# Performance work log

Hardware: AMD Instinct MI355X
Metric: run time of the kernel (lower is better)

Reference implementation:

```python
import jax, jax.numpy as jnp
import numpy as np

N_BAND = 5  # module hardcodes self.n = 5 -> keeps |i-j| <= N_BAND-1 = 4


def setup_inputs() -> dict:
    key = jax.random.key(0)
    ks = jax.random.split(key, 6)
    B, L, H = 4, 2048, 1024
    s = 1.0 / np.sqrt(H)
    return {
        "q": jax.random.normal(ks[0], (B, L, H), jnp.float32),
        "k": jax.random.normal(ks[1], (B, L, H), jnp.float32),
        "Wq": jax.random.normal(ks[2], (H, H), jnp.float32) * s,
        "bq": jax.random.normal(ks[3], (H,), jnp.float32) * s,
        "Wk": jax.random.normal(ks[4], (H, H), jnp.float32) * s,
        "bk": jax.random.normal(ks[5], (H,), jnp.float32) * s,
    }


def reference(q, k, Wq, bq, Wk, bk):
    b, l, e = q.shape
    # nn.Linear: y = x @ W^T + b
    qs = jnp.einsum("ble,he->blh", q, Wq) + bq
    ks = jnp.einsum("ble,he->blh", k, Wk) + bk
    # dense QK^T logits, [b, l, l]
    logits = jnp.einsum("blh,bmh->blm", qs, ks)
    # banded mask: the torch loop zeroes offsets 0..n-1 on both sides -> |i-j| <= n-1
    idx = jnp.arange(l)
    band = jnp.abs(idx[:, None] - idx[None, :]) <= (N_BAND - 1)  # [l, l]
    neg_inf = jnp.array(-jnp.inf, dtype=logits.dtype)
    logits = jnp.where(band[None, :, :], logits, neg_inf)
    # every row contains its diagonal, so softmax is well-defined
    return jax.nn.softmax(logits, axis=-1)
```

## Files before the change

kernel.cpp:

```cpp
#include <hip/hip_runtime.h>
#include <math.h>

#define LSEQ 2048
#define HDIM 1024
#define BATCH 4
#define ROWS (BATCH * LSEQ)
#define NBAND 9

typedef __attribute__((ext_vector_type(8))) short bf16x8;
typedef __attribute__((ext_vector_type(4))) float f32x4;
typedef __attribute__((ext_vector_type(8))) unsigned short u16x8;
typedef __attribute__((ext_vector_type(4))) unsigned uintx4;

#define AS3 __attribute__((address_space(3)))
#define AS1 __attribute__((address_space(1)))

__device__ __forceinline__ void gload16(const void* gp, void* lp) {
    __builtin_amdgcn_global_load_lds((AS1 const unsigned*)gp, (AS3 unsigned*)lp, 16, 0, 0);
}

__device__ __forceinline__ unsigned short f2bf(float x) {
    unsigned u = __float_as_uint(x);
    u += 0x7FFFu + ((u >> 16) & 1u);
    return (unsigned short)(u >> 16);
}
__device__ __forceinline__ float bf2f(unsigned short h) {
    return __uint_as_float(((unsigned)h) << 16);
}

__device__ __forceinline__ void split8(float4 a, float4 b, bf16x8& hi, bf16x8& lo) {
    float v[8] = {a.x, a.y, a.z, a.w, b.x, b.y, b.z, b.w};
#pragma unroll
    for (int j = 0; j < 8; j++) {
        unsigned short h = f2bf(v[j]);
        hi[j] = (short)h;
        lo[j] = (short)f2bf(v[j] - bf2f(h));
    }
}

__device__ __forceinline__ void unpack8(uintx4 w0, uintx4 w1, bf16x8& hi, bf16x8& lo) {
    union { bf16x8 v; uintx4 u; } H, L;
    H.u[0] = __builtin_amdgcn_perm(w0[1], w0[0], 0x05040100u);
    H.u[1] = __builtin_amdgcn_perm(w0[3], w0[2], 0x05040100u);
    H.u[2] = __builtin_amdgcn_perm(w1[1], w1[0], 0x05040100u);
    H.u[3] = __builtin_amdgcn_perm(w1[3], w1[2], 0x05040100u);
    L.u[0] = __builtin_amdgcn_perm(w0[1], w0[0], 0x07060302u);
    L.u[1] = __builtin_amdgcn_perm(w0[3], w0[2], 0x07060302u);
    L.u[2] = __builtin_amdgcn_perm(w1[1], w1[0], 0x07060302u);
    L.u[3] = __builtin_amdgcn_perm(w1[3], w1[2], 0x07060302u);
    hi = H.v; lo = L.v;
}

__global__ __launch_bounds__(256) void tcw_kernel(const float* __restrict__ Wq,
                                                  const float* __restrict__ Wk,
                                                  const float* __restrict__ bq,
                                                  unsigned short* __restrict__ qhi,
                                                  unsigned short* __restrict__ qlo,
                                                  unsigned short* __restrict__ khi,
                                                  unsigned short* __restrict__ klo,
                                                  float* __restrict__ wpart) {
    const int z = blockIdx.z;
    const int tid = threadIdx.x;
    if (z == 2) {
        const int fid = blockIdx.y * 16 + blockIdx.x;
        if (fid >= 64) return;
        const int c0 = tid * 4;
        float4 acc = {0.f, 0.f, 0.f, 0.f};
#pragma unroll
        for (int hh = 0; hh < 16; hh++) {
            const int h = fid * 16 + hh;
            const float s = bq[h];
            float4 v = *reinterpret_cast<const float4*>(&Wk[(size_t)h * HDIM + c0]);
            acc.x += v.x * s; acc.y += v.y * s; acc.z += v.z * s; acc.w += v.w * s;
        }
        *reinterpret_cast<float4*>(&wpart[(size_t)fid * HDIM + c0]) = acc;
        return;
    }
    __shared__ float tile[64][65];
    const float* src = z ? Wk : Wq;
    unsigned short* dh = z ? khi : qhi;
    unsigned short* dl = z ? klo : qlo;
    const int n0 = blockIdx.x * 64;
    const int h0 = blockIdx.y * 64;

#pragma unroll
    for (int p = 0; p < 4; p++) {
        const int h = p * 16 + (tid >> 4);
        const int n = (tid & 15) * 4;
        float4 v = *reinterpret_cast<const float4*>(&src[(size_t)(h0 + h) * HDIM + n0 + n]);
        tile[h][n + 0] = v.x; tile[h][n + 1] = v.y; tile[h][n + 2] = v.z; tile[h][n + 3] = v.w;
    }
    __syncthreads();
#pragma unroll
    for (int p = 0; p < 2; p++) {
        const int n = p * 32 + (tid >> 3);
        const int h = (tid & 7) * 8;
        u16x8 hv, lv;
#pragma unroll
        for (int j = 0; j < 8; j++) {
            float x = tile[h + j][n];
            unsigned short hb = f2bf(x);
            hv[j] = hb;
            lv[j] = f2bf(x - bf2f(hb));
        }
        *reinterpret_cast<u16x8*>(&dh[(size_t)(n0 + n) * HDIM + h0 + h]) = hv;
        *reinterpret_cast<u16x8*>(&dl[(size_t)(n0 + n) * HDIM + h0 + h]) = lv;
    }
}

__global__ __launch_bounds__(256) void convert_k_beta(const float* __restrict__ k,
                                                      const float* __restrict__ w,
                                                      unsigned short* __restrict__ Xhi,
                                                      unsigned short* __restrict__ Xlo,
                                                      float* __restrict__ beta) {
    __shared__ float red[4];
    const int r = blockIdx.x;
    const int t = threadIdx.x;
    float4 v = *reinterpret_cast<const float4*>(&k[(size_t)r * HDIM + t * 4]);
    float4 wv = *reinterpret_cast<const float4*>(&w[t * 4]);
    ushort4 h, l;
    h.x = f2bf(v.x); l.x = f2bf(v.x - bf2f(h.x));
    h.y = f2bf(v.y); l.y = f2bf(v.y - bf2f(h.y));
    h.z = f2bf(v.z); l.z = f2bf(v.z - bf2f(h.z));
    h.w = f2bf(v.w); l.w = f2bf(v.w - bf2f(h.w));
    reinterpret_cast<ushort4*>(Xhi)[(size_t)r * 256 + t] = h;
    reinterpret_cast<ushort4*>(Xlo)[(size_t)r * 256 + t] = l;
    float d = v.x * wv.x + v.y * wv.y + v.z * wv.z + v.w * wv.w;
#pragma unroll
    for (int off = 32; off > 0; off >>= 1) d += __shfl_xor(d, off, 64);
    if ((t & 63) == 0) red[t >> 6] = d;
    __syncthreads();
    if (t == 0) beta[r] = red[0] + red[1] + red[2] + red[3];
}

__global__ __launch_bounds__(256, 2) void gemm_part(
        const unsigned short* __restrict__ Ahi, const unsigned short* __restrict__ Alo,
        const unsigned short* __restrict__ Bhi, const unsigned short* __restrict__ Blo,
        float* __restrict__ Cparts) {
    __shared__ unsigned short sh[4 * 4096];
    const int AHI = 0, ALO = 4096, BHI = 8192, BLO = 12288;
    const int tid = threadIdx.x;
    const int w = tid >> 6, l = tid & 63;
    const int wr = w >> 1, wc = w & 1;
    const int row0 = blockIdx.x * 128, col0 = blockIdx.y * 128;
    const int kbeg = blockIdx.z * 256;
    float* C = Cparts + (size_t)blockIdx.z * HDIM * HDIM;
    const int srow0 = (l >> 2), scbp = l & 3;

    f32x4 acc[4][4];
#pragma unroll
    for (int m = 0; m < 4; m++)
#pragma unroll
        for (int n = 0; n < 4; n++) acc[m][n] = (f32x4){0.f, 0.f, 0.f, 0.f};

    const int fr_a[4] = {wr * 64 + (l & 15), wr * 64 + 16 + (l & 15),
                         wr * 64 + 32 + (l & 15), wr * 64 + 48 + (l & 15)};
    const int fr_b[4] = {wc * 64 + (l & 15), wc * 64 + 16 + (l & 15),
                         wc * 64 + 32 + (l & 15), wc * 64 + 48 + (l & 15)};
    const int cb = l >> 4;

    for (int k0 = kbeg; k0 < kbeg + 256; k0 += 32) {
#pragma unroll
        for (int i = 0; i < 2; i++) {
            const int seg = i * 4 + w;
            const int row = seg * 16 + srow0;
            const int cbs = scbp ^ ((row >> 1) & 3);
            gload16(Ahi + (size_t)(row0 + row) * HDIM + k0 + cbs * 8, &sh[AHI + seg * 512]);
            gload16(Alo + (size_t)(row0 + row) * HDIM + k0 + cbs * 8, &sh[ALO + seg * 512]);
            gload16(Bhi + (size_t)(col0 + row) * HDIM + k0 + cbs * 8, &sh[BHI + seg * 512]);
            gload16(Blo + (size_t)(col0 + row) * HDIM + k0 + cbs * 8, &sh[BLO + seg * 512]);
        }
        __syncthreads();

        bf16x8 ah[4], al[4], bh[4], bl[4];
#pragma unroll
        for (int m = 0; m < 4; m++) {
            const int r = fr_a[m];
            const int cbs = cb ^ ((r >> 1) & 3);
            ah[m] = *reinterpret_cast<const bf16x8*>(&sh[AHI + r * 32 + cbs * 8]);
            al[m] = *reinterpret_cast<const bf16x8*>(&sh[ALO + r * 32 + cbs * 8]);
        }
#pragma unroll
        for (int n = 0; n < 4; n++) {
            const int r = fr_b[n];
            const int cbs = cb ^ ((r >> 1) & 3);
            bh[n] = *reinterpret_cast<const bf16x8*>(&sh[BHI + r * 32 + cbs * 8]);
            bl[n] = *reinterpret_cast<const bf16x8*>(&sh[BLO + r * 32 + cbs * 8]);
        }
#pragma unroll
        for (int m = 0; m < 4; m++)
#pragma unroll
            for (int n = 0; n < 4; n++) {
                acc[m][n] = __builtin_amdgcn_mfma_f32_16x16x32_bf16(ah[m], bh[n], acc[m][n], 0, 0, 0);
                acc[m][n] = __builtin_amdgcn_mfma_f32_16x16x32_bf16(ah[m], bl[n], acc[m][n], 0, 0, 0);
                acc[m][n] = __builtin_amdgcn_mfma_f32_16x16x32_bf16(al[m], bh[n], acc[m][n], 0, 0, 0);
            }
        __syncthreads();
    }

    const int lcol = l & 15, lrow = (l >> 4) * 4;
#pragma unroll
    for (int n = 0; n < 4; n++) {
        const int colg = col0 + wc * 64 + n * 16 + lcol;
#pragma unroll
        for (int m = 0; m < 4; m++) {
            const int rowg = row0 + wr * 64 + m * 16 + lrow;
#pragma unroll
            for (int v = 0; v < 4; v++)
                C[(size_t)(rowg + v) * HDIM + colg] = acc[m][n][v];
        }
    }
}

__global__ __launch_bounds__(256) void reduceMw_convert(const float* __restrict__ Mparts,
                                                        unsigned short* __restrict__ Mhi,
                                                        unsigned short* __restrict__ Mlo,
                                                        const float* __restrict__ wpart,
                                                        float* __restrict__ w) {
    if (blockIdx.x >= 1024) {
        const int c = (blockIdx.x - 1024) * 256 + threadIdx.x;
        float s = 0.f;
#pragma unroll
        for (int b = 0; b < 64; b++) s += wpart[(size_t)b * HDIM + c];
        w[c] = s;
        return;
    }
    const int idx4 = blockIdx.x * 256 + threadIdx.x;
    float4 s = {0.f, 0.f, 0.f, 0.f};
#pragma unroll
    for (int z = 0; z < 4; z++) {
        float4 v = reinterpret_cast<const float4*>(Mparts + (size_t)z * HDIM * HDIM)[idx4];
        s.x += v.x; s.y += v.y; s.z += v.z; s.w += v.w;
    }
    ushort4 h, l;
    h.x = f2bf(s.x); l.x = f2bf(s.x - bf2f(h.x));
    h.y = f2bf(s.y); l.y = f2bf(s.y - bf2f(h.y));
    h.z = f2bf(s.z); l.z = f2bf(s.z - bf2f(h.z));
    h.w = f2bf(s.w); l.w = f2bf(s.w - bf2f(h.w));
    reinterpret_cast<ushort4*>(Mhi)[idx4] = h;
    reinterpret_cast<ushort4*>(Mlo)[idx4] = l;
}

__global__ __launch_bounds__(512, 2) void gemm_t(
        const unsigned short* __restrict__ Ahi, const unsigned short* __restrict__ Alo,
        const unsigned short* __restrict__ Bhi, const unsigned short* __restrict__ Blo,
        unsigned* __restrict__ Tpack) {
    __shared__ unsigned short sh[2][24576];
    const int AHI = 0, ALO = 8192, BHI = 16384, BLO = 20480;
    const int tid = threadIdx.x;
    const int w = tid >> 6, l = tid & 63;
    const int wr = w >> 1, wc = w & 1;
    const int row0 = blockIdx.x * 256, col0 = blockIdx.y * 128;
    const int srow0 = (l >> 2), scbp = l & 3;

    f32x4 acc[4][4];
#pragma unroll
    for (int m = 0; m < 4; m++)
#pragma unroll
        for (int n = 0; n < 4; n++) acc[m][n] = (f32x4){0.f, 0.f, 0.f, 0.f};

    const int fr_a[4] = {wr * 64 + (l & 15), wr * 64 + 16 + (l & 15),
                         wr * 64 + 32 + (l & 15), wr * 64 + 48 + (l & 15)};
    const int fr_b[4] = {wc * 64 + (l & 15), wc * 64 + 16 + (l & 15),
                         wc * 64 + 32 + (l & 15), wc * 64 + 48 + (l & 15)};
    const int cb = l >> 4;

    auto stage = [&](int buf, int k0) {
#pragma unroll
        for (int i = 0; i < 2; i++) {
            const int seg = i * 8 + w;
            const int row = seg * 16 + srow0;
            const int cbs = scbp ^ ((row >> 1) & 3);
            gload16(Ahi + (size_t)(row0 + row) * HDIM + k0 + cbs * 8, &sh[buf][AHI + seg * 512]);
            gload16(Alo + (size_t)(row0 + row) * HDIM + k0 + cbs * 8, &sh[buf][ALO + seg * 512]);
        }
        {
            const int seg = w;
            const int row = seg * 16 + srow0;
            const int cbs = scbp ^ ((row >> 1) & 3);
            gload16(Bhi + (size_t)(col0 + row) * HDIM + k0 + cbs * 8, &sh[buf][BHI + seg * 512]);
            gload16(Blo + (size_t)(col0 + row) * HDIM + k0 + cbs * 8, &sh[buf][BLO + seg * 512]);
        }
    };
    auto compute = [&](int buf) {
        bf16x8 ah[4], al[4], bh[4], bl[4];
#pragma unroll
        for (int m = 0; m < 4; m++) {
            const int r = fr_a[m];
            const int cbs = cb ^ ((r >> 1) & 3);
            ah[m] = *reinterpret_cast<const bf16x8*>(&sh[buf][AHI + r * 32 + cbs * 8]);
            al[m] = *reinterpret_cast<const bf16x8*>(&sh[buf][ALO + r * 32 + cbs * 8]);
        }
#pragma unroll
        for (int n = 0; n < 4; n++) {
            const int r = fr_b[n];
            const int cbs = cb ^ ((r >> 1) & 3);
            bh[n] = *reinterpret_cast<const bf16x8*>(&sh[buf][BHI + r * 32 + cbs * 8]);
            bl[n] = *reinterpret_cast<const bf16x8*>(&sh[buf][BLO + r * 32 + cbs * 8]);
        }
#pragma unroll
        for (int m = 0; m < 4; m++)
#pragma unroll
            for (int n = 0; n < 4; n++) {
                acc[m][n] = __builtin_amdgcn_mfma_f32_16x16x32_bf16(ah[m], bh[n], acc[m][n], 0, 0, 0);
                acc[m][n] = __builtin_amdgcn_mfma_f32_16x16x32_bf16(ah[m], bl[n], acc[m][n], 0, 0, 0);
                acc[m][n] = __builtin_amdgcn_mfma_f32_16x16x32_bf16(al[m], bh[n], acc[m][n], 0, 0, 0);
            }
    };

    stage(0, 0);
    __syncthreads();
    int cur = 0;
    for (int t = 0; t < 31; t++) {
        stage(cur ^ 1, (t + 1) * 32);
        compute(cur);
        __syncthreads();
        cur ^= 1;
    }
    compute(cur);

    const int lcol = l & 15, lrow = (l >> 4) * 4;
#pragma unroll
    for (int n = 0; n < 4; n++) {
        const int colg = col0 + wc * 64 + n * 16 + lcol;
#pragma unroll
        for (int m = 0; m < 4; m++) {
            const int rowg = row0 + wr * 64 + m * 16 + lrow;
#pragma unroll
            for (int v = 0; v < 4; v++) {
                const float x = acc[m][n][v];
                const unsigned short h = f2bf(x);
                const unsigned short lo = f2bf(x - bf2f(h));
                Tpack[(size_t)(rowg + v) * HDIM + colg] = (unsigned)h | ((unsigned)lo << 16);
            }
        }
    }
}

__global__ __launch_bounds__(256) void band_mfma(const float* __restrict__ q,
                                                 const unsigned* __restrict__ tpack,
                                                 const float* __restrict__ beta,
                                                 float* __restrict__ band) {
    __shared__ float lds_c[4][16][33];
    const int tid = threadIdx.x;
    const int w = tid >> 6, l = tid & 63;
    const int r0 = blockIdx.x * 16;
    const int b = r0 >> 11;
    const int i0 = r0 & (LSEQ - 1);
    const int fr = l & 15;
    const int kb = (l >> 4) * 8;

    const float* qrow = q + (size_t)(r0 + fr) * HDIM;
    const size_t tb = (size_t)b * LSEQ * HDIM;

    const int j0 = i0 - 4 + fr;
    const int j1 = i0 + 12 + fr;
    const int j0c = min(max(j0, 0), LSEQ - 1);
    const int j1c = min(max(j1, 0), LSEQ - 1);
    const bool v0 = (j0 >= 0) && (j0 < LSEQ);
    const bool v1 = (j1 >= 0) && (j1 < LSEQ);
    const bool interior = (i0 >= 4) && (i0 + 19 < LSEQ);
    const uintx4 uz = {0u, 0u, 0u, 0u};

    f32x4 c0 = {0.f, 0.f, 0.f, 0.f};
    f32x4 c1 = {0.f, 0.f, 0.f, 0.f};

#pragma unroll 2
    for (int ks = 0; ks < 8; ks++) {
        const int k0 = w * 256 + ks * 32 + kb;
        float4 qa = *reinterpret_cast<const float4*>(qrow + k0);
        float4 qb = *reinterpret_cast<const float4*>(qrow + k0 + 4);
        uintx4 w00 = *reinterpret_cast<const uintx4*>(&tpack[tb + (size_t)j0c * HDIM + k0]);
        uintx4 w01 = *reinterpret_cast<const uintx4*>(&tpack[tb + (size_t)j0c * HDIM + k0 + 4]);
        uintx4 w10 = *reinterpret_cast<const uintx4*>(&tpack[tb + (size_t)j1c * HDIM + k0]);
        uintx4 w11 = *reinterpret_cast<const uintx4*>(&tpack[tb + (size_t)j1c * HDIM + k0 + 4]);
        if (!interior) {
            if (!v0) { w00 = uz; w01 = uz; }
            if (!v1) { w10 = uz; w11 = uz; }
        }
        bf16x8 ah, al, b0h, b0l, b1h, b1l;
        split8(qa, qb, ah, al);
        unpack8(w00, w01, b0h, b0l);
        unpack8(w10, w11, b1h, b1l);
        c0 = __builtin_amdgcn_mfma_f32_16x16x32_bf16(ah, b0h, c0, 0, 0, 0);
        c0 = __builtin_amdgcn_mfma_f32_16x16x32_bf16(ah, b0l, c0, 0, 0, 0);
        c0 = __builtin_amdgcn_mfma_f32_16x16x32_bf16(al, b0h, c0, 0, 0, 0);
        c1 = __builtin_amdgcn_mfma_f32_16x16x32_bf16(ah, b1h, c1, 0, 0, 0);
        c1 = __builtin_amdgcn_mfma_f32_16x16x32_bf16(ah, b1l, c1, 0, 0, 0);
        c1 = __builtin_amdgcn_mfma_f32_16x16x32_bf16(al, b1h, c1, 0, 0, 0);
    }

#pragma unroll
    for (int v = 0; v < 4; v++) {
        lds_c[w][(l >> 4) * 4 + v][fr] = c0[v];
        lds_c[w][(l >> 4) * 4 + v][16 + fr] = c1[v];
    }
    __syncthreads();

#pragma unroll
    for (int e = tid; e < 512; e += 256) {
        const int rr = e >> 5, cc = e & 31;
        lds_c[0][rr][cc] = lds_c[0][rr][cc] + lds_c[1][rr][cc] +
                           lds_c[2][rr][cc] + lds_c[3][rr][cc];
    }
    __syncthreads();

    if (tid < 16) {
        const int il = i0 + tid;
        const int ig = r0 + tid;
        float lg[NBAND];
#pragma unroll
        for (int d = 0; d < NBAND; d++) {
            const int j = il + d - 4;
            lg[d] = (j >= 0 && j < LSEQ)
                    ? lds_c[0][tid][tid + d] + beta[(size_t)b * LSEQ + j]
                    : -1e30f;
        }
        float m = -1e30f;
#pragma unroll
        for (int d = 0; d < NBAND; d++) m = fmaxf(m, lg[d]);
        float p[NBAND], s = 0.f;
#pragma unroll
        for (int d = 0; d < NBAND; d++) { p[d] = expf(lg[d] - m); s += p[d]; }
        const float inv = 1.f / s;
#pragma unroll
        for (int d = 0; d < NBAND; d++) band[(size_t)ig * NBAND + d] = p[d] * inv;
    }
}

__global__ __launch_bounds__(256) void expand_band(const float* __restrict__ band,
                                                   float* __restrict__ out) {
    const size_t idx4 = (size_t)blockIdx.x * 256 + threadIdx.x;
    const size_t flat = idx4 * 4;
    const int j0 = (int)(flat & (LSEQ - 1));
    const size_t row = flat >> 11;
    const int i = (int)(row & (LSEQ - 1));
    float v[4];
#pragma unroll
    for (int s = 0; s < 4; s++) {
        const int dj = (j0 + s) - i + 4;
        v[s] = (dj >= 0 && dj < NBAND) ? band[row * NBAND + dj] : 0.f;
    }
    float4 o = {v[0], v[1], v[2], v[3]};
    *reinterpret_cast<float4*>(&out[flat]) = o;
}

__global__ __launch_bounds__(256) void gemm_nt_bias(const float* __restrict__ A,
                                                    const float* __restrict__ B,
                                                    const float* __restrict__ bias,
                                                    float* __restrict__ C) {
    __shared__ float As[8][132];
    __shared__ float Bs[8][132];
    const int tid = threadIdx.x;
    const int row0 = blockIdx.x * 128, col0 = blockIdx.y * 128;
    const int lr = tid >> 1, lc = (tid & 1) * 4;
    const int tx = tid & 15, ty = tid >> 4;
    float acc[2][2][4][4];
#pragma unroll
    for (int a = 0; a < 2; a++)
#pragma unroll
        for (int b = 0; b < 2; b++)
#pragma unroll
            for (int c = 0; c < 4; c++)
#pragma unroll
                for (int d = 0; d < 4; d++) acc[a][b][c][d] = 0.f;
    for (int k0 = 0; k0 < HDIM; k0 += 8) {
        float4 av = *reinterpret_cast<const float4*>(&A[(size_t)(row0 + lr) * HDIM + k0 + lc]);
        float4 bv = *reinterpret_cast<const float4*>(&B[(size_t)(col0 + lr) * HDIM + k0 + lc]);
        __syncthreads();
        As[lc + 0][lr] = av.x; As[lc + 1][lr] = av.y; As[lc + 2][lr] = av.z; As[lc + 3][lr] = av.w;
        Bs[lc + 0][lr] = bv.x; Bs[lc + 1][lr] = bv.y; Bs[lc + 2][lr] = bv.z; Bs[lc + 3][lr] = bv.w;
        __syncthreads();
#pragma unroll
        for (int kk = 0; kk < 8; kk++) {
            float4 a0 = *reinterpret_cast<const float4*>(&As[kk][ty * 4]);
            float4 a1 = *reinterpret_cast<const float4*>(&As[kk][64 + ty * 4]);
            float4 b0 = *reinterpret_cast<const float4*>(&Bs[kk][tx * 4]);
            float4 b1 = *reinterpret_cast<const float4*>(&Bs[kk][64 + tx * 4]);
            float am[2][4] = {{a0.x, a0.y, a0.z, a0.w}, {a1.x, a1.y, a1.z, a1.w}};
            float bw[2][4] = {{b0.x, b0.y, b0.z, b0.w}, {b1.x, b1.y, b1.z, b1.w}};
#pragma unroll
            for (int mi = 0; mi < 2; mi++)
#pragma unroll
                for (int ni = 0; ni < 2; ni++)
#pragma unroll
                    for (int mm = 0; mm < 4; mm++)
#pragma unroll
                        for (int nn = 0; nn < 4; nn++)
                            acc[mi][ni][mm][nn] += am[mi][mm] * bw[ni][nn];
        }
    }
#pragma unroll
    for (int mi = 0; mi < 2; mi++)
#pragma unroll
        for (int mm = 0; mm < 4; mm++) {
            const int r = row0 + mi * 64 + ty * 4 + mm;
#pragma unroll
            for (int ni = 0; ni < 2; ni++) {
                const int c = col0 + ni * 64 + tx * 4;
                float4 o;
                o.x = acc[mi][ni][mm][0] + bias[c + 0];
                o.y = acc[mi][ni][mm][1] + bias[c + 1];
                o.z = acc[mi][ni][mm][2] + bias[c + 2];
                o.w = acc[mi][ni][mm][3] + bias[c + 3];
                *reinterpret_cast<float4*>(&C[(size_t)r * HDIM + c]) = o;
            }
        }
}

__global__ __launch_bounds__(256) void band_softmax(const float* __restrict__ qs,
                                                    const float* __restrict__ ks,
                                                    float* __restrict__ band) {
    const int wave = threadIdx.x >> 6;
    const int lane = threadIdx.x & 63;
    const int r = blockIdx.x * 4 + wave;
    const int b = r >> 11;
    const int i = r & (LSEQ - 1);
    const float* qrow = qs + (size_t)r * HDIM;
    const float* kbase = ks + (size_t)b * LSEQ * HDIM;
    float acc[NBAND];
#pragma unroll
    for (int d = 0; d < NBAND; d++) acc[d] = 0.f;
    for (int h = lane; h < HDIM; h += 64) {
        const float qv = qrow[h];
#pragma unroll
        for (int d = 0; d < NBAND; d++) {
            const int j = i + d - 4;
            if (j >= 0 && j < LSEQ)
                acc[d] += qv * kbase[(size_t)j * HDIM + h];
        }
    }
#pragma unroll
    for (int d = 0; d < NBAND; d++) {
        float v = acc[d];
#pragma unroll
        for (int off = 32; off > 0; off >>= 1) v += __shfl_xor(v, off, 64);
        acc[d] = v;
    }
    if (lane == 0) {
        float m = -1e30f;
#pragma unroll
        for (int d = 0; d < NBAND; d++) {
            const int j = i + d - 4;
            if (j >= 0 && j < LSEQ) m = fmaxf(m, acc[d]);
        }
        float p[NBAND];
        float s = 0.f;
#pragma unroll
        for (int d = 0; d < NBAND; d++) {
            const int j = i + d - 4;
            p[d] = (j >= 0 && j < LSEQ) ? expf(acc[d] - m) : 0.f;
            s += p[d];
        }
        const float inv = 1.f / s;
#pragma unroll
        for (int d = 0; d < NBAND; d++) band[(size_t)r * NBAND + d] = p[d] * inv;
    }
}

extern "C" void kernel_launch(void* const* d_in, const int* in_sizes, int n_in,
                              void* d_out, int out_size, void* d_ws, size_t ws_size,
                              hipStream_t stream) {
    const float* q  = (const float*)d_in[0];
    const float* k  = (const float*)d_in[1];
    const float* Wq = (const float*)d_in[2];
    const float* bq = (const float*)d_in[3];
    const float* Wk = (const float*)d_in[4];
    const float* bk = (const float*)d_in[5];
    float* out = (float*)d_out;

    const size_t bandB = (size_t)ROWS * NBAND * sizeof(float);
    char* p = (char*)d_ws;
    float* band = (float*)p;                 p += bandB;
    unsigned short* Xhi = (unsigned short*)p; p += (size_t)ROWS * HDIM * 2;
    unsigned short* Xlo = (unsigned short*)p; p += (size_t)ROWS * HDIM * 2;
    unsigned short* Mhi = (unsigned short*)p; p += (size_t)HDIM * HDIM * 2;
    unsigned short* Mlo = (unsigned short*)p; p += (size_t)HDIM * HDIM * 2;
    float* w        = (float*)p;             p += HDIM * sizeof(float);
    float* wpart    = (float*)p;             p += 64 * HDIM * sizeof(float);
    float* beta     = (float*)p;             p += ROWS * sizeof(float);
    const size_t need = (size_t)(p - (char*)d_ws);

    unsigned short* WqTh = Xhi;
    unsigned short* WqTl = Xhi + (size_t)HDIM * HDIM;
    unsigned short* WkTh = Xhi + 2 * (size_t)HDIM * HDIM;
    unsigned short* WkTl = Xhi + 3 * (size_t)HDIM * HDIM;

    unsigned* tpack = (unsigned*)out;
    float* Mparts = (float*)((char*)out + 32ull * 1024 * 1024);

    if (ws_size >= need) {
        dim3 tg(16, 16, 3);
        tcw_kernel<<<tg, 256, 0, stream>>>(Wq, Wk, bq, WqTh, WqTl, WkTh, WkTl, wpart);
        dim3 mg(8, 8, 4);
        gemm_part<<<mg, 256, 0, stream>>>(WqTh, WqTl, WkTh, WkTl, Mparts);
        reduceMw_convert<<<1028, 256, 0, stream>>>(Mparts, Mhi, Mlo, wpart, w);
        convert_k_beta<<<ROWS, 256, 0, stream>>>(k, w, Xhi, Xlo, beta);
        dim3 gg(ROWS / 256, HDIM / 128);
        gemm_t<<<gg, 512, 0, stream>>>(Xhi, Xlo, Mhi, Mlo, tpack);
        band_mfma<<<ROWS / 16, 256, 0, stream>>>(q, tpack, beta, band);
        expand_band<<<(size_t)ROWS * LSEQ / 4 / 256, 256, 0, stream>>>(band, out);
    } else {
        float* qs = out;
        float* ks = out + (size_t)ROWS * HDIM;
        dim3 gg(ROWS / 128, HDIM / 128);
        gemm_nt_bias<<<gg, 256, 0, stream>>>(q, Wq, bq, qs);
        gemm_nt_bias<<<gg, 256, 0, stream>>>(k, Wk, bk, ks);
        band_softmax<<<ROWS / 4, 256, 0, stream>>>(qs, ks, band);
        expand_band<<<(size_t)ROWS * LSEQ / 4 / 256, 256, 0, stream>>>(band, out);
    }
}
```

Measured before the change: 133.1 us.

## Fuse band softmax with dense output expansion and shrink gemm_t tile

Adds a band_fuse kernel that computes the banded softmax and then writes the full dense output rows for its 16-row block directly. This removes the separate expand_band launch and the band buffer round trip. To make that possible, the intermediate tpack buffer moves from the output into workspace when the workspace is large enough. gemm_t also drops from 512 threads and 256-row tiles to 256 threads and 128-row tiles, which doubles the grid and lowers data reuse per block.

```diff
diff --git a/kernel.cpp b/kernel.cpp
--- a/kernel.cpp
+++ b/kernel.cpp
@@ -241,16 +241,16 @@
     reinterpret_cast<ushort4*>(Mlo)[idx4] = l;
 }
 
-__global__ __launch_bounds__(512, 2) void gemm_t(
+__global__ __launch_bounds__(256, 2) void gemm_t(
         const unsigned short* __restrict__ Ahi, const unsigned short* __restrict__ Alo,
         const unsigned short* __restrict__ Bhi, const unsigned short* __restrict__ Blo,
         unsigned* __restrict__ Tpack) {
-    __shared__ unsigned short sh[2][24576];
-    const int AHI = 0, ALO = 8192, BHI = 16384, BLO = 20480;
+    __shared__ unsigned short sh[2][16384];
+    const int AHI = 0, ALO = 4096, BHI = 8192, BLO = 12288;
     const int tid = threadIdx.x;
     const int w = tid >> 6, l = tid & 63;
     const int wr = w >> 1, wc = w & 1;
-    const int row0 = blockIdx.x * 256, col0 = blockIdx.y * 128;
+    const int row0 = blockIdx.x * 128, col0 = blockIdx.y * 128;
     const int srow0 = (l >> 2), scbp = l & 3;
 
     f32x4 acc[4][4];
@@ -268,16 +268,11 @@
     auto stage = [&](int buf, int k0) {
 #pragma unroll
         for (int i = 0; i < 2; i++) {
-            const int seg = i * 8 + w;
+            const int seg = i * 4 + w;
             const int row = seg * 16 + srow0;
             const int cbs = scbp ^ ((row >> 1) & 3);
             gload16(Ahi + (size_t)(row0 + row) * HDIM + k0 + cbs * 8, &sh[buf][AHI + seg * 512]);
             gload16(Alo + (size_t)(row0 + row) * HDIM + k0 + cbs * 8, &sh[buf][ALO + seg * 512]);
-        }
-        {
-            const int seg = w;
-            const int row = seg * 16 + srow0;
-            const int cbs = scbp ^ ((row >> 1) & 3);
             gload16(Bhi + (size_t)(col0 + row) * HDIM + k0 + cbs * 8, &sh[buf][BHI + seg * 512]);
             gload16(Blo + (size_t)(col0 + row) * HDIM + k0 + cbs * 8, &sh[buf][BLO + seg * 512]);
         }
@@ -337,16 +332,11 @@
     }
 }
 
-__global__ __launch_bounds__(256) void band_mfma(const float* __restrict__ q,
-                                                 const unsigned* __restrict__ tpack,
-                                                 const float* __restrict__ beta,
-                                                 float* __restrict__ band) {
-    __shared__ float lds_c[4][16][33];
-    const int tid = threadIdx.x;
+__device__ __forceinline__ void band_core(const float* __restrict__ q,
+                                          const unsigned* __restrict__ tpack,
+                                          int r0, int b, int i0, int tid,
+                                          float (*lds_c)[16][33]) {
     const int w = tid >> 6, l = tid & 63;
-    const int r0 = blockIdx.x * 16;
-    const int b = r0 >> 11;
-    const int i0 = r0 & (LSEQ - 1);
     const int fr = l & 15;
     const int kb = (l >> 4) * 8;
 
@@ -404,6 +394,18 @@
                            lds_c[2][rr][cc] + lds_c[3][rr][cc];
     }
     __syncthreads();
+}
+
+__global__ __launch_bounds__(256) void band_mfma(const float* __restrict__ q,
+                                                 const unsigned* __restrict__ tpack,
+                                                 const float* __restrict__ beta,
+                                                 float* __restrict__ band) {
+    __shared__ float lds_c[4][16][33];
+    const int tid = threadIdx.x;
+    const int r0 = blockIdx.x * 16;
+    const int b = r0 >> 11;
+    const int i0 = r0 & (LSEQ - 1);
+    band_core(q, tpack, r0, b, i0, tid, lds_c);
 
     if (tid < 16) {
         const int il = i0 + tid;
@@ -425,6 +427,55 @@
         const float inv = 1.f / s;
 #pragma unroll
         for (int d = 0; d < NBAND; d++) band[(size_t)ig * NBAND + d] = p[d] * inv;
+    }
+}
+
+__global__ __launch_bounds__(256) void band_fuse(const float* __restrict__ q,
+                                                 const unsigned* __restrict__ tpack,
+                                                 const float* __restrict__ beta,
+                                                 float* __restrict__ out) {
+    __shared__ float lds_c[4][16][33];
+    const int tid = threadIdx.x;
+    const int r0 = blockIdx.x * 16;
+    const int b = r0 >> 11;
+    const int i0 = r0 & (LSEQ - 1);
+    band_core(q, tpack, r0, b, i0, tid, lds_c);
+
+    float* pr = &lds_c[1][0][0];
+    if (tid < 16) {
+        const int il = i0 + tid;
+        float lg[NBAND];
+#pragma unroll
+        for (int d = 0; d < NBAND; d++) {
+            const int j = il + d - 4;
+            lg[d] = (j >= 0 && j < LSEQ)
+                    ? lds_c[0][tid][tid + d] + beta[(size_t)b * LSEQ + j]
+                    : -1e30f;
+        }
+        float m = -1e30f;
+#pragma unroll
+        for (int d = 0; d < NBAND; d++) m = fmaxf(m, lg[d]);
+        float p[NBAND], s = 0.f;
+#pragma unroll
+        for (int d = 0; d < NBAND; d++) { p[d] = expf(lg[d] - m); s += p[d]; }
+        const float inv = 1.f / s;
+#pragma unroll
+        for (int d = 0; d < NBAND; d++) pr[tid * NBAND + d] = p[d] * inv;
+    }
+    __syncthreads();
+
+    for (int e = tid; e < 8192; e += 256) {
+        const int rr = e >> 9;
+        const int c0 = (e & 511) * 4;
+        const int il = i0 + rr;
+        float v[4];
+#pragma unroll
+        for (int s = 0; s < 4; s++) {
+            const int dj = c0 + s - il + 4;
+            v[s] = (dj >= 0 && dj < NBAND) ? pr[rr * NBAND + dj] : 0.f;
+        }
+        float4 o = {v[0], v[1], v[2], v[3]};
+        *reinterpret_cast<float4*>(&out[(size_t)(r0 + rr) * LSEQ + c0]) = o;
     }
 }
 
@@ -580,13 +631,14 @@
     float* wpart    = (float*)p;             p += 64 * HDIM * sizeof(float);
     float* beta     = (float*)p;             p += ROWS * sizeof(float);
     const size_t need = (size_t)(p - (char*)d_ws);
+    const size_t tpackOff = (need + 255) & ~(size_t)255;
+    const size_t need2 = tpackOff + (size_t)ROWS * HDIM * sizeof(unsigned);
 
     unsigned short* WqTh = Xhi;
     unsigned short* WqTl = Xhi + (size_t)HDIM * HDIM;
     unsigned short* WkTh = Xhi + 2 * (size_t)HDIM * HDIM;
     unsigned short* WkTl = Xhi + 3 * (size_t)HDIM * HDIM;
 
-    unsigned* tpack = (unsigned*)out;
     float* Mparts = (float*)((char*)out + 32ull * 1024 * 1024);
 
     if (ws_size >= need) {
@@ -596,10 +648,17 @@
         gemm_part<<<mg, 256, 0, stream>>>(WqTh, WqTl, WkTh, WkTl, Mparts);
         reduceMw_convert<<<1028, 256, 0, stream>>>(Mparts, Mhi, Mlo, wpart, w);
         convert_k_beta<<<ROWS, 256, 0, stream>>>(k, w, Xhi, Xlo, beta);
-        dim3 gg(ROWS / 256, HDIM / 128);
-        gemm_t<<<gg, 512, 0, stream>>>(Xhi, Xlo, Mhi, Mlo, tpack);
-        band_mfma<<<ROWS / 16, 256, 0, stream>>>(q, tpack, beta, band);
-        expand_band<<<(size_t)ROWS * LSEQ / 4 / 256, 256, 0, stream>>>(band, out);
+        dim3 gg(ROWS / 128, HDIM / 128);
+        if (ws_size >= need2) {
+            unsigned* tpack = (unsigned*)((char*)d_ws + tpackOff);
+            gemm_t<<<gg, 256, 0, stream>>>(Xhi, Xlo, Mhi, Mlo, tpack);
+            band_fuse<<<ROWS / 16, 256, 0, stream>>>(q, tpack, beta, out);
+        } else {
+            unsigned* tpack = (unsigned*)out;
+            gemm_t<<<gg, 256, 0, stream>>>(Xhi, Xlo, Mhi, Mlo, tpack);
+            band_mfma<<<ROWS / 16, 256, 0, stream>>>(q, tpack, beta, band);
+            expand_band<<<(size_t)ROWS * LSEQ / 4 / 256, 256, 0, stream>>>(band, out);
+        }
     } else {
         float* qs = out;
         float* ks = out + (size_t)ROWS * HDIM;
```

After: 130.1 us. 2.3% less time.
